# Performance work log

Hardware: AMD Instinct MI355X
Metric: run time of the kernel (lower is better)

Reference implementation:

```python
import jax, jax.numpy as jnp
import numpy as np

B, T, D = 4, 2048, 2048
H = 16
KD = D // 2          # key_dim = expand_k * d_model
VD = D               # value_dim = expand_v * d_model
DK = KD // H         # head_k_dim = 64
DV = VD // H         # head_v_dim = 128
LR = 16              # gate_low_rank_dim
EPS = 1e-5
GATE_LOGIT_NORMALIZER = 16.0


def setup_inputs() -> dict:
    key = jax.random.key(0)
    ks = jax.random.split(key, 9)
    def w(k, shape):
        fan_in = shape[0]
        return (jax.random.normal(k, shape, jnp.float32) * (fan_in ** -0.5)).astype(jnp.float32)
    return {
        "x":      jax.random.normal(ks[0], (B, T, D), jnp.float32),
        "Wq":     w(ks[1], (D, KD)),
        "Wk":     w(ks[2], (D, KD)),
        "Wv":     w(ks[3], (D, VD)),
        "Wg":     w(ks[4], (D, VD)),      # output gate projection
        "Wgk1":   w(ks[5], (D, LR)),      # gk low-rank down-proj (no bias)
        "Wgk2":   w(ks[6], (LR, KD)),     # gk up-proj
        "bgk2":   jnp.zeros((KD,), jnp.float32),
        "norm_w": jnp.ones((DV,), jnp.float32),  # per-head RMSNorm weight
        "Wo":     w(ks[7], (VD, D)),
    }


def reference(x, Wq, Wk, Wv, Wg, Wgk1, Wgk2, bgk2, norm_w, Wo):
    b, t, _ = x.shape
    dv = norm_w.shape[0]
    vd = Wv.shape[1]
    h = vd // dv
    dk = Wq.shape[1] // h
    scale = dk ** -0.5

    q = (x @ Wq).reshape(b, t, h, dk) * scale
    k = (x @ Wk).reshape(b, t, h, dk)
    v = (x @ Wv).reshape(b, t, h, dv)
    # forget gate: logsigmoid(low_rank_proj(x)) / gate_logit_normalizer
    gk = jax.nn.log_sigmoid((x @ Wgk1) @ Wgk2 + bgk2) / GATE_LOGIT_NORMALIZER
    gk = gk.reshape(b, t, h, dk)

    # time-major for scan: [T, B, H, d]
    qT = jnp.moveaxis(q, 1, 0)
    kT = jnp.moveaxis(k, 1, 0)
    vT = jnp.moveaxis(v, 1, 0)
    gT = jnp.moveaxis(gk, 1, 0)

    def step(S, inp):
        qt, kt, vt, gt = inp
        # S_t = diag(exp(gk_t)) S_{t-1} + k_t^T v_t ; shape [B,H,DK,DV]
        S = S * jnp.exp(gt)[..., None] + kt[..., None] * vt[..., None, :]
        ot = jnp.einsum('bhk,bhkv->bhv', qt, S)
        return S, ot

    S0 = jnp.zeros((b, h, dk, dv), x.dtype)
    _, o = jax.lax.scan(step, S0, (qT, kT, vT, gT))
    o = jnp.moveaxis(o, 0, 1)  # [B, T, H, DV]

    # FusedRMSNormSwishGate: rmsnorm(o) * weight * swish(g), per head dim
    g = (x @ Wg).reshape(b, t, h, dv)
    o = o * jax.lax.rsqrt(jnp.mean(o * o, axis=-1, keepdims=True) + EPS) * norm_w
    o = o * (g * jax.nn.sigmoid(g))
    return o.reshape(b, t, vd) @ Wo
```

## Files before the change

kernel.cpp:

```cpp
#include <hip/hip_runtime.h>
#include <hip/hip_bf16.h>
#include <type_traits>


using bf16x8 = __attribute__((ext_vector_type(8))) short;
using f32x4  = __attribute__((ext_vector_type(4))) float;

static __device__ __forceinline__ float bf2f(ushort u) {
  union { unsigned int i; float f; } v;
  v.i = ((unsigned int)u) << 16;
  return v.f;
}
static __device__ __forceinline__ ushort f2bf(float f) {
  __hip_bfloat16 h = __float2bfloat16(f);
  return *reinterpret_cast<ushort*>(&h);
}
static __device__ __forceinline__ unsigned int pack2(float lo, float hi) {
  return (unsigned int)f2bf(lo) | ((unsigned int)f2bf(hi) << 16);
}
static __device__ __forceinline__ void unpack8(uint4 v, float* f) {
  f[0] = bf2f((ushort)(v.x & 0xffff)); f[1] = bf2f((ushort)(v.x >> 16));
  f[2] = bf2f((ushort)(v.y & 0xffff)); f[3] = bf2f((ushort)(v.y >> 16));
  f[4] = bf2f((ushort)(v.z & 0xffff)); f[5] = bf2f((ushort)(v.z >> 16));
  f[6] = bf2f((ushort)(v.w & 0xffff)); f[7] = bf2f((ushort)(v.w >> 16));
}

#define GLDS16(g, l) __builtin_amdgcn_global_load_lds( \
    (const __attribute__((address_space(1))) unsigned int*)(g), \
    (__attribute__((address_space(3))) unsigned int*)(l), 16, 0, 0)

#define SWZ3(row) ((((row) & 1) << 2) | (((row) >> 1) & 3))

__global__ __launch_bounds__(256) void f32_to_bf16(
    const float* __restrict__ in, ushort* __restrict__ out, long n) {
  long i = ((long)blockIdx.x * 256 + threadIdx.x) * 8;
  if (i >= n) return;
  float4 a = *(const float4*)(in + i);
  float4 b = *(const float4*)(in + i + 4);
  uint4 o;
  o.x = pack2(a.x, a.y); o.y = pack2(a.z, a.w);
  o.z = pack2(b.x, b.y); o.w = pack2(b.z, b.w);
  *(uint4*)(out + i) = o;
}

__global__ __launch_bounds__(256) void transpose_f32_bf16(
    const float* __restrict__ in, ushort* __restrict__ out, int R, int C) {
  __shared__ float tile[64][65];
  const int t = threadIdx.x;
  const int tc = blockIdx.x * 64;
  const int tr = blockIdx.y * 64;
  const int lr = t >> 2;
  const int lc = (t & 3) * 16;
  const float* ip = in + (long)(tr + lr) * C + tc + lc;
#pragma unroll
  for (int j = 0; j < 4; ++j)
    *(float4*)(&tile[lr][lc + j * 4]) = *(const float4*)(ip + j * 4);
  __syncthreads();
  const int c = t >> 2;
  const int r0 = (t & 3) * 16;
  ushort tmp[16];
#pragma unroll
  for (int j = 0; j < 16; ++j) tmp[j] = f2bf(tile[r0 + j][c]);
  ushort* op = out + (long)(tc + c) * R + tr + r0;
  *(uint4*)(op)     = *(uint4*)(tmp);
  *(uint4*)(op + 8) = *(uint4*)(tmp + 8);
}

template <typename OT>
__global__ __launch_bounds__(512, 2) void gemm_bt8(
    const ushort* __restrict__ A, const ushort* __restrict__ BT,
    OT* __restrict__ C, int M, int N, int K) {
  __shared__ ushort sA[2 * 16384];
  __shared__ ushort sB[2 * 16384];
  const int t = threadIdx.x;
  const int nbx = N >> 8;
  const int cpx = gridDim.x >> 3;
  const int wg = ((int)blockIdx.x & 7) * cpx + ((int)blockIdx.x >> 3);
  const int brow = (wg / nbx) * 256;
  const int bcol = (wg % nbx) * 256;

  const int w = t >> 6, l = t & 63;
  const int wm = w >> 2, wn = w & 3;
  const int lr = l & 15, lk = l >> 4;
  const int NT = K >> 6;

  const int srow = t >> 3;
  const int cswz = ((t & 7) ^ SWZ3(srow)) * 8;
  const ushort* Abase = A + (size_t)(brow + srow) * K + cswz;
  const ushort* Bbase = BT + (size_t)(bcol + srow) * K + cswz;
  const int t8 = t * 8;

  auto stageA = [&](int bb, int hh, int jt) {
    const ushort* s = Abase + (size_t)(hh * 128) * K + jt * 64;
    ushort* d = sA + bb * 16384 + hh * 8192 + t8;
    GLDS16(s, d);
    GLDS16(s + (size_t)64 * K, d + 4096);
  };
  auto stageB = [&](int bb, int hh, int jt) {
    const ushort* s = Bbase + (size_t)(hh * 128) * K + jt * 64;
    ushort* d = sB + bb * 16384 + hh * 8192 + t8;
    GLDS16(s, d);
    GLDS16(s + (size_t)64 * K, d + 4096);
  };

  const int swz = SWZ3(lr);
  const int ks0 = ((0 + lk) ^ swz) * 8;
  const int ks1 = ((4 + lk) ^ swz) * 8;
  const int aRd = (wm * 16 + lr) * 64;
  const int bRd = (wn * 16 + lr) * 64;

  f32x4 acc[8][4];
#pragma unroll
  for (int m = 0; m < 8; ++m)
#pragma unroll
    for (int n = 0; n < 4; ++n) acc[m][n] = (f32x4){0.f, 0.f, 0.f, 0.f};

  stageA(0, 0, 0); stageB(0, 0, 0); stageB(0, 1, 0); stageA(0, 1, 0);
  asm volatile("s_waitcnt vmcnt(4)" ::: "memory");
  stageA(1, 0, 1); stageB(1, 0, 1); stageB(1, 1, 1);
  asm volatile("s_waitcnt vmcnt(6)" ::: "memory");
  __builtin_amdgcn_s_barrier();

  for (int kt = 0; kt < NT; ++kt) {
    const int bb = kt & 1;
    const int aOff = bb * 16384, bOff = bb * 16384;
    bf16x8 aF[4][2], bF[2][2][2];

#pragma unroll
    for (int m = 0; m < 4; ++m) {
      aF[m][0] = *(const bf16x8*)(sA + aOff + aRd + m * 2048 + ks0);
      aF[m][1] = *(const bf16x8*)(sA + aOff + aRd + m * 2048 + ks1);
    }
#pragma unroll
    for (int n = 0; n < 2; ++n) {
      bF[0][n][0] = *(const bf16x8*)(sB + bOff + bRd + n * 4096 + ks0);
      bF[0][n][1] = *(const bf16x8*)(sB + bOff + bRd + n * 4096 + ks1);
    }
    if (kt + 1 < NT) stageA(bb ^ 1, 1, kt + 1);
    __builtin_amdgcn_s_barrier();
    __builtin_amdgcn_s_setprio(1);
#pragma unroll
    for (int m = 0; m < 4; ++m)
#pragma unroll
      for (int n = 0; n < 2; ++n) {
        acc[m][n] = __builtin_amdgcn_mfma_f32_16x16x32_bf16(aF[m][0], bF[0][n][0], acc[m][n], 0, 0, 0);
        acc[m][n] = __builtin_amdgcn_mfma_f32_16x16x32_bf16(aF[m][1], bF[0][n][1], acc[m][n], 0, 0, 0);
      }
    __builtin_amdgcn_s_setprio(0);
    __builtin_amdgcn_s_barrier();

#pragma unroll
    for (int n = 0; n < 2; ++n) {
      bF[1][n][0] = *(const bf16x8*)(sB + bOff + 8192 + bRd + n * 4096 + ks0);
      bF[1][n][1] = *(const bf16x8*)(sB + bOff + 8192 + bRd + n * 4096 + ks1);
    }
    if (kt + 2 < NT) stageA(bb, 0, kt + 2);
    __builtin_amdgcn_s_barrier();
    __builtin_amdgcn_s_setprio(1);
#pragma unroll
    for (int m = 0; m < 4; ++m)
#pragma unroll
      for (int n = 0; n < 2; ++n) {
        acc[m][2 + n] = __builtin_amdgcn_mfma_f32_16x16x32_bf16(aF[m][0], bF[1][n][0], acc[m][2 + n], 0, 0, 0);
        acc[m][2 + n] = __builtin_amdgcn_mfma_f32_16x16x32_bf16(aF[m][1], bF[1][n][1], acc[m][2 + n], 0, 0, 0);
      }
    __builtin_amdgcn_s_setprio(0);
    __builtin_amdgcn_s_barrier();

#pragma unroll
    for (int m = 0; m < 4; ++m) {
      aF[m][0] = *(const bf16x8*)(sA + aOff + 8192 + aRd + m * 2048 + ks0);
      aF[m][1] = *(const bf16x8*)(sA + aOff + 8192 + aRd + m * 2048 + ks1);
    }
    if (kt + 2 < NT) stageB(bb, 0, kt + 2);
    __builtin_amdgcn_s_barrier();
    __builtin_amdgcn_s_setprio(1);
#pragma unroll
    for (int m = 0; m < 4; ++m)
#pragma unroll
      for (int n = 0; n < 2; ++n) {
        acc[4 + m][n] = __builtin_amdgcn_mfma_f32_16x16x32_bf16(aF[m][0], bF[0][n][0], acc[4 + m][n], 0, 0, 0);
        acc[4 + m][n] = __builtin_amdgcn_mfma_f32_16x16x32_bf16(aF[m][1], bF[0][n][1], acc[4 + m][n], 0, 0, 0);
      }
    __builtin_amdgcn_s_setprio(0);
    __builtin_amdgcn_s_barrier();

    if (kt + 2 < NT) stageB(bb, 1, kt + 2);
    __builtin_amdgcn_s_barrier();
    __builtin_amdgcn_s_setprio(1);
#pragma unroll
    for (int m = 0; m < 4; ++m)
#pragma unroll
      for (int n = 0; n < 2; ++n) {
        acc[4 + m][2 + n] = __builtin_amdgcn_mfma_f32_16x16x32_bf16(aF[m][0], bF[1][n][0], acc[4 + m][2 + n], 0, 0, 0);
        acc[4 + m][2 + n] = __builtin_amdgcn_mfma_f32_16x16x32_bf16(aF[m][1], bF[1][n][1], acc[4 + m][2 + n], 0, 0, 0);
      }
    __builtin_amdgcn_s_setprio(0);
    if (kt < NT - 2)       asm volatile("s_waitcnt vmcnt(6)" ::: "memory");
    else if (kt == NT - 2) asm volatile("s_waitcnt vmcnt(0)" ::: "memory");
    __builtin_amdgcn_s_barrier();
  }

  const int rq = lk * 4;
#pragma unroll
  for (int mq = 0; mq < 8; ++mq)
#pragma unroll
    for (int nq = 0; nq < 4; ++nq) {
      long row = brow + mq * 32 + wm * 16 + rq;
      long col = bcol + nq * 64 + wn * 16 + lr;
      OT* cp = C + row * N + col;
#pragma unroll
      for (int r = 0; r < 4; ++r) {
        if constexpr (std::is_same_v<OT, ushort>) cp[(long)r * N] = f2bf(acc[mq][nq][r]);
        else                                      cp[(long)r * N] = acc[mq][nq][r];
      }
    }
}

__global__ __launch_bounds__(256) void gate_kernel(
    const float* __restrict__ x, const float* __restrict__ Wgk1,
    const float* __restrict__ Wgk2, const float* __restrict__ bgk2,
    ushort* __restrict__ gbuf) {
  const int m = blockIdx.x;
  const int t = threadIdx.x;
  __shared__ float sx[2048];
  __shared__ float red[256];
  __shared__ float z1[16];
  const float* xr = x + (long)m * 2048;
  *(float4*)(sx + t * 8)     = *(const float4*)(xr + t * 8);
  *(float4*)(sx + t * 8 + 4) = *(const float4*)(xr + t * 8 + 4);
  __syncthreads();
  const int j = t & 15, seg = t >> 4;
  float s = 0.f;
  for (int d = 0; d < 128; ++d)
    s += sx[seg * 128 + d] * Wgk1[(seg * 128 + d) * 16 + j];
  red[t] = s;
  __syncthreads();
  if (t < 16) {
    float z = 0.f;
    for (int sg = 0; sg < 16; ++sg) z += red[sg * 16 + t];
    z1[t] = z;
  }
  __syncthreads();
#pragma unroll
  for (int r = 0; r < 4; ++r) {
    int n = r * 256 + t;
    float a = bgk2[n];
#pragma unroll
    for (int l2 = 0; l2 < 16; ++l2) a += z1[l2] * Wgk2[l2 * 1024 + n];
    float ls = fminf(a, 0.f) - log1pf(__expf(-fabsf(a)));
    gbuf[(long)m * 1024 + n] = f2bf(ls * 0.0625f);
  }
}

__global__ __launch_bounds__(256) void chunk_contrib_kernel(
    const ushort* __restrict__ qkvg, const ushort* __restrict__ gbuf,
    float* __restrict__ Sall, float* __restrict__ Gtot) {
  const int blk = blockIdx.x;
  const int bh = blk >> 5, c = blk & 31;
  const int b = bh >> 4, h = bh & 15;
  const long row0 = (long)b * 2048 + c * 64;
  const int th = threadIdx.x;

  __shared__ float  gc[64][65];
  __shared__ ushort khT[64][72];
  __shared__ ushort vT[128][72];

  {
    const int t = th >> 2;
    const int k0 = (th & 3) * 16;
    const ushort* gp = gbuf + (row0 + t) * 1024 + h * 64 + k0;
    uint4 a = *(const uint4*)gp;
    uint4 b4 = *(const uint4*)(gp + 8);
    float f[8];
    unpack8(a, f);
#pragma unroll
    for (int j = 0; j < 8; ++j) gc[t][k0 + j] = f[j];
    unpack8(b4, f);
#pragma unroll
    for (int j = 0; j < 8; ++j) gc[t][k0 + 8 + j] = f[j];
  }
  __syncthreads();
  if (th < 64) {
    float s = 0.f;
    for (int t = 0; t < 64; ++t) { s += gc[t][th]; gc[t][th] = s; }
  }
  __syncthreads();
  if (th < 64) Gtot[(long)blk * 64 + th] = gc[63][th];

  {
    const int s = th & 63, kq = th >> 6;
    const ushort* kp = qkvg + (row0 + s) * 6144 + 1024 + h * 64 + kq * 16;
    uint4 a = *(const uint4*)kp;
    uint4 b4 = *(const uint4*)(kp + 8);
    float f[16];
    unpack8(a, f); unpack8(b4, f + 8);
#pragma unroll
    for (int j = 0; j < 16; ++j) {
      int k = kq * 16 + j;
      khT[k][s] = f2bf(f[j] * __expf(gc[63][k] - gc[s][k]));
    }
    const ushort* vp = qkvg + (row0 + s) * 6144 + 2048 + h * 128 + kq * 32;
#pragma unroll
    for (int u = 0; u < 4; ++u) {
      uint4 vv = *(const uint4*)(vp + u * 8);
      const ushort* pv = (const ushort*)&vv;
#pragma unroll
      for (int j = 0; j < 8; ++j) vT[kq * 32 + u * 8 + j][s] = pv[j];
    }
  }
  __syncthreads();

  const int w = th >> 6, l = th & 63;
  const int lr = l & 15, kq8 = (l >> 4) * 8;
  f32x4 acc[4][2];
#pragma unroll
  for (int m = 0; m < 4; ++m)
#pragma unroll
    for (int n = 0; n < 2; ++n) acc[m][n] = (f32x4){0.f, 0.f, 0.f, 0.f};
#pragma unroll
  for (int ks = 0; ks < 64; ks += 32) {
#pragma unroll
    for (int m = 0; m < 4; ++m) {
      bf16x8 af = *(const bf16x8*)(&khT[m * 16 + lr][ks + kq8]);
#pragma unroll
      for (int n = 0; n < 2; ++n) {
        bf16x8 bv = *(const bf16x8*)(&vT[w * 32 + n * 16 + lr][ks + kq8]);
        acc[m][n] = __builtin_amdgcn_mfma_f32_16x16x32_bf16(af, bv, acc[m][n], 0, 0, 0);
      }
    }
  }
  float* Cc = Sall + (long)blk * 8192;
  const int rq = (l >> 4) * 4;
#pragma unroll
  for (int m = 0; m < 4; ++m)
#pragma unroll
    for (int n = 0; n < 2; ++n) {
      int k = m * 16 + rq;
      int dv = w * 32 + n * 16 + lr;
#pragma unroll
      for (int r = 0; r < 4; ++r) Cc[(k + r) * 128 + dv] = acc[m][n][r];
    }
}

__global__ __launch_bounds__(256) void chunk_scan_kernel(
    float* __restrict__ Sall, const float* __restrict__ Gtot) {
  const int blk = blockIdx.x;
  const int bh = blk >> 2, qd = blk & 3;
  const int th = threadIdx.x;
  const int k = th >> 2;
  const int dv = qd * 32 + (th & 3) * 8;
  float* base = Sall + (long)bh * 32 * 8192 + k * 128 + dv;
  const float* gt = Gtot + (long)bh * 32 * 64 + k;
  float S[8];
#pragma unroll
  for (int i = 0; i < 8; ++i) S[i] = 0.f;
  for (int c = 0; c < 32; ++c) {
    float4 c0 = *(const float4*)(base);
    float4 c1 = *(const float4*)(base + 4);
    float eg = __expf(gt[c * 64]);
    float4 s0 = {S[0], S[1], S[2], S[3]};
    float4 s1 = {S[4], S[5], S[6], S[7]};
    *(float4*)(base) = s0;
    *(float4*)(base + 4) = s1;
    S[0] = S[0] * eg + c0.x; S[1] = S[1] * eg + c0.y;
    S[2] = S[2] * eg + c0.z; S[3] = S[3] * eg + c0.w;
    S[4] = S[4] * eg + c1.x; S[5] = S[5] * eg + c1.y;
    S[6] = S[6] * eg + c1.z; S[7] = S[7] * eg + c1.w;
    base += 8192;
  }
}

__global__ __launch_bounds__(256) void chunk_output_kernel(
    const ushort* __restrict__ qkvg, const ushort* __restrict__ gbuf,
    const float* __restrict__ Sall, const float* __restrict__ norm_w,
    ushort* __restrict__ oo) {
  const int blk = blockIdx.x;
  const int bh = blk >> 5, c = blk & 31;
  const int b = bh >> 4, h = bh & 15;
  const long row0 = (long)b * 2048 + c * 64;
  const int th = threadIdx.x;

  __shared__ float  gc[64][65];
  __shared__ ushort qg[64][72];
  __shared__ ushort kg[64][72];
  __shared__ ushort vT[128][72];
  __shared__ ushort ST[128][72];
  __shared__ ushort P[64][72];
  __shared__ ushort ot[64][136];

  {
    const int t = th >> 2;
    const int s4 = (th & 3);
    const int k0 = s4 * 16;
    const ushort* gp = gbuf + (row0 + t) * 1024 + h * 64 + k0;
    uint4 a = *(const uint4*)gp;
    uint4 b4 = *(const uint4*)(gp + 8);
    float f[8];
    unpack8(a, f);
#pragma unroll
    for (int j = 0; j < 8; ++j) gc[t][k0 + j] = f[j];
    unpack8(b4, f);
#pragma unroll
    for (int j = 0; j < 8; ++j) gc[t][k0 + 8 + j] = f[j];

    const ushort* qp = qkvg + (row0 + t) * 6144 + h * 64 + k0;
    *(uint4*)(&qg[t][k0])     = *(const uint4*)qp;
    *(uint4*)(&qg[t][k0 + 8]) = *(const uint4*)(qp + 8);
    const ushort* kp = qp + 1024;
    *(uint4*)(&kg[t][k0])     = *(const uint4*)kp;
    *(uint4*)(&kg[t][k0 + 8]) = *(const uint4*)(kp + 8);

    const ushort* gtp = qkvg + (row0 + t) * 6144 + 4096 + h * 128 + s4 * 32;
#pragma unroll
    for (int u = 0; u < 4; ++u)
      *(uint4*)(&ot[t][s4 * 32 + u * 8]) = *(const uint4*)(gtp + u * 8);
  }
  {
    const int s = th & 63, kq = th >> 6;
    const ushort* vp = qkvg + (row0 + s) * 6144 + 2048 + h * 128 + kq * 32;
#pragma unroll
    for (int u = 0; u < 4; ++u) {
      uint4 vv = *(const uint4*)(vp + u * 8);
      const ushort* pv = (const ushort*)&vv;
#pragma unroll
      for (int j = 0; j < 8; ++j) vT[kq * 32 + u * 8 + j][s] = pv[j];
    }
  }
  {
    const int k = th >> 2;
    const int dvb = (th & 3) * 32;
    const float* sp = Sall + (long)blk * 8192 + k * 128 + dvb;
#pragma unroll
    for (int u = 0; u < 8; ++u) {
      float4 sv = *(const float4*)(sp + u * 4);
      ST[dvb + u * 4 + 0][k] = f2bf(sv.x);
      ST[dvb + u * 4 + 1][k] = f2bf(sv.y);
      ST[dvb + u * 4 + 2][k] = f2bf(sv.z);
      ST[dvb + u * 4 + 3][k] = f2bf(sv.w);
    }
  }
  __syncthreads();
  if (th < 64) {
    float s = 0.f;
    for (int t = 0; t < 64; ++t) { s += gc[t][th]; gc[t][th] = s; }
  }
  __syncthreads();
  {
    const int t = th & 63, kb = (th >> 6) * 16;
#pragma unroll
    for (int u = 0; u < 2; ++u) {
      uint4 qv = *(const uint4*)(&qg[t][kb + u * 8]);
      uint4 kv = *(const uint4*)(&kg[t][kb + u * 8]);
      float qf[8], kf[8];
      unpack8(qv, qf); unpack8(kv, kf);
      ushort qo[8], ko[8];
#pragma unroll
      for (int j = 0; j < 8; ++j) {
        float g = gc[t][kb + u * 8 + j];
        qo[j] = f2bf(qf[j] * __expf(g) * 0.125f);
        ko[j] = f2bf(kf[j] * __expf(-g));
      }
      *(uint4*)(&qg[t][kb + u * 8]) = *(uint4*)qo;
      *(uint4*)(&kg[t][kb + u * 8]) = *(uint4*)ko;
    }
  }
  __syncthreads();

  const int w = th >> 6, l = th & 63;
  const int lr = l & 15, kq8 = (l >> 4) * 8;
  const int rq = (l >> 4) * 4;

  f32x4 acc1[4];
#pragma unroll
  for (int n = 0; n < 4; ++n) acc1[n] = (f32x4){0.f, 0.f, 0.f, 0.f};
#pragma unroll
  for (int kk = 0; kk < 64; kk += 32) {
    bf16x8 af = *(const bf16x8*)(&qg[w * 16 + lr][kk + kq8]);
#pragma unroll
    for (int n = 0; n < 4; ++n) {
      bf16x8 bv = *(const bf16x8*)(&kg[n * 16 + lr][kk + kq8]);
      acc1[n] = __builtin_amdgcn_mfma_f32_16x16x32_bf16(af, bv, acc1[n], 0, 0, 0);
    }
  }
#pragma unroll
  for (int n = 0; n < 4; ++n) {
    int s = n * 16 + lr;
#pragma unroll
    for (int r = 0; r < 4; ++r) {
      int t = w * 16 + rq + r;
      P[t][s] = f2bf(s <= t ? acc1[n][r] : 0.f);
    }
  }
  __syncthreads();

  f32x4 acc2[8];
#pragma unroll
  for (int n = 0; n < 8; ++n) acc2[n] = (f32x4){0.f, 0.f, 0.f, 0.f};
#pragma unroll
  for (int ks = 0; ks < 64; ks += 32) {
    bf16x8 af = *(const bf16x8*)(&P[w * 16 + lr][ks + kq8]);
#pragma unroll
    for (int n = 0; n < 8; ++n) {
      bf16x8 bv = *(const bf16x8*)(&vT[n * 16 + lr][ks + kq8]);
      acc2[n] = __builtin_amdgcn_mfma_f32_16x16x32_bf16(af, bv, acc2[n], 0, 0, 0);
    }
  }
#pragma unroll
  for (int kk = 0; kk < 64; kk += 32) {
    bf16x8 af = *(const bf16x8*)(&qg[w * 16 + lr][kk + kq8]);
#pragma unroll
    for (int n = 0; n < 8; ++n) {
      bf16x8 bv = *(const bf16x8*)(&ST[n * 16 + lr][kk + kq8]);
      acc2[n] = __builtin_amdgcn_mfma_f32_16x16x32_bf16(af, bv, acc2[n], 0, 0, 0);
    }
  }

  float sumsq[4] = {0.f, 0.f, 0.f, 0.f};
#pragma unroll
  for (int n = 0; n < 8; ++n)
#pragma unroll
    for (int r = 0; r < 4; ++r) sumsq[r] += acc2[n][r] * acc2[n][r];
#pragma unroll
  for (int d = 1; d < 16; d <<= 1)
#pragma unroll
    for (int r = 0; r < 4; ++r) sumsq[r] += __shfl_xor(sumsq[r], d);
  float inv[4];
#pragma unroll
  for (int r = 0; r < 4; ++r) inv[r] = rsqrtf(sumsq[r] * (1.f / 128.f) + 1e-5f);

#pragma unroll
  for (int n = 0; n < 8; ++n) {
    int dv = n * 16 + lr;
    float nw = norm_w[dv];
#pragma unroll
    for (int r = 0; r < 4; ++r) {
      int t = w * 16 + rq + r;
      float g = bf2f(ot[t][dv]);
      float sw = g / (1.f + __expf(-g));
      ot[t][dv] = f2bf(acc2[n][r] * inv[r] * nw * sw);
    }
  }
  __syncthreads();

  {
    const int row = th >> 2;
    const int col0 = (th & 3) * 32;
    ushort* op = oo + (row0 + row) * 2048 + h * 128 + col0;
#pragma unroll
    for (int u = 0; u < 4; ++u)
      *(uint4*)(op + u * 8) = *(const uint4*)(&ot[row][col0 + u * 8]);
  }
}

extern "C" void kernel_launch(void* const* d_in, const int* in_sizes, int n_in,
                              void* d_out, int out_size, void* d_ws, size_t ws_size,
                              hipStream_t stream) {
  const float* x      = (const float*)d_in[0];
  const float* Wq     = (const float*)d_in[1];
  const float* Wk     = (const float*)d_in[2];
  const float* Wv     = (const float*)d_in[3];
  const float* Wg     = (const float*)d_in[4];
  const float* Wgk1   = (const float*)d_in[5];
  const float* Wgk2   = (const float*)d_in[6];
  const float* bgk2   = (const float*)d_in[7];
  const float* norm_w = (const float*)d_in[8];
  const float* Wo     = (const float*)d_in[9];
  float* out = (float*)d_out;

  char* ws = (char*)d_ws;
  ushort* WT   = (ushort*)(ws);
  ushort* WoT  = (ushort*)(ws + 25165824);
  ushort* qkvg = (ushort*)(ws + 33554432);
  ushort* gbuf = (ushort*)(ws + 134217728);
  float*  Sall = (float*)(ws + 150994944);
  ushort* xb   = (ushort*)(ws + 150994944);
  float*  Gtot = (float*)(ws + 218103808);
  ushort* oo   = (ushort*)(ws + 218628096);

  dim3 blk(256);
  f32_to_bf16<<<dim3(8192), blk, 0, stream>>>(x, xb, (long)8192 * 2048);
  transpose_f32_bf16<<<dim3(16, 32), blk, 0, stream>>>(Wq, WT, 2048, 1024);
  transpose_f32_bf16<<<dim3(16, 32), blk, 0, stream>>>(Wk, WT + (size_t)1024 * 2048, 2048, 1024);
  transpose_f32_bf16<<<dim3(32, 32), blk, 0, stream>>>(Wv, WT + (size_t)2048 * 2048, 2048, 2048);
  transpose_f32_bf16<<<dim3(32, 32), blk, 0, stream>>>(Wg, WT + (size_t)4096 * 2048, 2048, 2048);
  transpose_f32_bf16<<<dim3(32, 32), blk, 0, stream>>>(Wo, WoT, 2048, 2048);

  gemm_bt8<ushort><<<dim3(768), dim3(512), 0, stream>>>(xb, WT, qkvg, 8192, 6144, 2048);
  gate_kernel<<<dim3(8192), blk, 0, stream>>>(x, Wgk1, Wgk2, bgk2, gbuf);

  chunk_contrib_kernel<<<dim3(2048), blk, 0, stream>>>(qkvg, gbuf, Sall, Gtot);
  chunk_scan_kernel<<<dim3(256), blk, 0, stream>>>(Sall, Gtot);
  chunk_output_kernel<<<dim3(2048), blk, 0, stream>>>(qkvg, gbuf, Sall, norm_w, oo);

  gemm_bt8<float><<<dim3(256), dim3(512), 0, stream>>>(oo, WoT, out, 8192, 2048, 2048);
}
```

Measured before the change: 523.7 us.

## Switch GEMM to 32x32 MFMA, store chunk states as transposed bf16, trim output kernel

Result: faster. 476.2 us (-9.1%).

```diff
diff --git a/kernel.cpp b/kernel.cpp
--- a/kernel.cpp
+++ b/kernel.cpp
@@ -5,6 +5,7 @@
 
 using bf16x8 = __attribute__((ext_vector_type(8))) short;
 using f32x4  = __attribute__((ext_vector_type(4))) float;
+using f32x16 = __attribute__((ext_vector_type(16))) float;
 
 static __device__ __forceinline__ float bf2f(ushort u) {
   union { unsigned int i; float f; } v;
@@ -81,7 +82,7 @@
 
   const int w = t >> 6, l = t & 63;
   const int wm = w >> 2, wn = w & 3;
-  const int lr = l & 15, lk = l >> 4;
+  const int l31 = l & 31, l5 = l >> 5;
   const int NT = K >> 6;
 
   const int srow = t >> 3;
@@ -103,17 +104,18 @@
     GLDS16(s + (size_t)64 * K, d + 4096);
   };
 
-  const int swz = SWZ3(lr);
-  const int ks0 = ((0 + lk) ^ swz) * 8;
-  const int ks1 = ((4 + lk) ^ swz) * 8;
-  const int aRd = (wm * 16 + lr) * 64;
-  const int bRd = (wn * 16 + lr) * 64;
-
-  f32x4 acc[8][4];
-#pragma unroll
-  for (int m = 0; m < 8; ++m)
-#pragma unroll
-    for (int n = 0; n < 4; ++n) acc[m][n] = (f32x4){0.f, 0.f, 0.f, 0.f};
+  const int swz = SWZ3(l31 & 7);
+  const int aRow = (wm * 32 + l31) * 64;
+  const int bRow = (wn * 32 + l31) * 64;
+#define KSL(ks) ((((ks) * 2 + l5) ^ swz) * 8)
+
+  f32x16 acc[4][2];
+#pragma unroll
+  for (int m = 0; m < 4; ++m)
+#pragma unroll
+    for (int n = 0; n < 2; ++n)
+#pragma unroll
+      for (int r = 0; r < 16; ++r) acc[m][n][r] = 0.f;
 
   stageA(0, 0, 0); stageB(0, 0, 0); stageB(0, 1, 0); stageA(0, 1, 0);
   asm volatile("s_waitcnt vmcnt(4)" ::: "memory");
@@ -124,64 +126,54 @@
   for (int kt = 0; kt < NT; ++kt) {
     const int bb = kt & 1;
     const int aOff = bb * 16384, bOff = bb * 16384;
-    bf16x8 aF[4][2], bF[2][2][2];
-
-#pragma unroll
-    for (int m = 0; m < 4; ++m) {
-      aF[m][0] = *(const bf16x8*)(sA + aOff + aRd + m * 2048 + ks0);
-      aF[m][1] = *(const bf16x8*)(sA + aOff + aRd + m * 2048 + ks1);
-    }
-#pragma unroll
-    for (int n = 0; n < 2; ++n) {
-      bF[0][n][0] = *(const bf16x8*)(sB + bOff + bRd + n * 4096 + ks0);
-      bF[0][n][1] = *(const bf16x8*)(sB + bOff + bRd + n * 4096 + ks1);
-    }
+    bf16x8 aF[2][4], bF[2][4];
+
+#pragma unroll
+    for (int mf = 0; mf < 2; ++mf)
+#pragma unroll
+      for (int ks = 0; ks < 4; ++ks)
+        aF[mf][ks] = *(const bf16x8*)(sA + aOff + mf * 4096 + aRow + KSL(ks));
+#pragma unroll
+    for (int ks = 0; ks < 4; ++ks)
+      bF[0][ks] = *(const bf16x8*)(sB + bOff + bRow + KSL(ks));
     if (kt + 1 < NT) stageA(bb ^ 1, 1, kt + 1);
     __builtin_amdgcn_s_barrier();
     __builtin_amdgcn_s_setprio(1);
 #pragma unroll
-    for (int m = 0; m < 4; ++m)
-#pragma unroll
-      for (int n = 0; n < 2; ++n) {
-        acc[m][n] = __builtin_amdgcn_mfma_f32_16x16x32_bf16(aF[m][0], bF[0][n][0], acc[m][n], 0, 0, 0);
-        acc[m][n] = __builtin_amdgcn_mfma_f32_16x16x32_bf16(aF[m][1], bF[0][n][1], acc[m][n], 0, 0, 0);
-      }
+    for (int mf = 0; mf < 2; ++mf)
+#pragma unroll
+      for (int ks = 0; ks < 4; ++ks)
+        acc[mf][0] = __builtin_amdgcn_mfma_f32_32x32x16_bf16(aF[mf][ks], bF[0][ks], acc[mf][0], 0, 0, 0);
     __builtin_amdgcn_s_setprio(0);
     __builtin_amdgcn_s_barrier();
 
 #pragma unroll
-    for (int n = 0; n < 2; ++n) {
-      bF[1][n][0] = *(const bf16x8*)(sB + bOff + 8192 + bRd + n * 4096 + ks0);
-      bF[1][n][1] = *(const bf16x8*)(sB + bOff + 8192 + bRd + n * 4096 + ks1);
-    }
+    for (int ks = 0; ks < 4; ++ks)
+      bF[1][ks] = *(const bf16x8*)(sB + bOff + 8192 + bRow + KSL(ks));
     if (kt + 2 < NT) stageA(bb, 0, kt + 2);
     __builtin_amdgcn_s_barrier();
     __builtin_amdgcn_s_setprio(1);
 #pragma unroll
-    for (int m = 0; m < 4; ++m)
-#pragma unroll
-      for (int n = 0; n < 2; ++n) {
-        acc[m][2 + n] = __builtin_amdgcn_mfma_f32_16x16x32_bf16(aF[m][0], bF[1][n][0], acc[m][2 + n], 0, 0, 0);
-        acc[m][2 + n] = __builtin_amdgcn_mfma_f32_16x16x32_bf16(aF[m][1], bF[1][n][1], acc[m][2 + n], 0, 0, 0);
-      }
+    for (int mf = 0; mf < 2; ++mf)
+#pragma unroll
+      for (int ks = 0; ks < 4; ++ks)
+        acc[mf][1] = __builtin_amdgcn_mfma_f32_32x32x16_bf16(aF[mf][ks], bF[1][ks], acc[mf][1], 0, 0, 0);
     __builtin_amdgcn_s_setprio(0);
     __builtin_amdgcn_s_barrier();
 
 #pragma unroll
-    for (int m = 0; m < 4; ++m) {
-      aF[m][0] = *(const bf16x8*)(sA + aOff + 8192 + aRd + m * 2048 + ks0);
-      aF[m][1] = *(const bf16x8*)(sA + aOff + 8192 + aRd + m * 2048 + ks1);
-    }
+    for (int mf = 0; mf < 2; ++mf)
+#pragma unroll
+      for (int ks = 0; ks < 4; ++ks)
+        aF[mf][ks] = *(const bf16x8*)(sA + aOff + 8192 + mf * 4096 + aRow + KSL(ks));
     if (kt + 2 < NT) stageB(bb, 0, kt + 2);
     __builtin_amdgcn_s_barrier();
     __builtin_amdgcn_s_setprio(1);
 #pragma unroll
-    for (int m = 0; m < 4; ++m)
-#pragma unroll
-      for (int n = 0; n < 2; ++n) {
-        acc[4 + m][n] = __builtin_amdgcn_mfma_f32_16x16x32_bf16(aF[m][0], bF[0][n][0], acc[4 + m][n], 0, 0, 0);
-        acc[4 + m][n] = __builtin_amdgcn_mfma_f32_16x16x32_bf16(aF[m][1], bF[0][n][1], acc[4 + m][n], 0, 0, 0);
-      }
+    for (int mf = 0; mf < 2; ++mf)
+#pragma unroll
+      for (int ks = 0; ks < 4; ++ks)
+        acc[2 + mf][0] = __builtin_amdgcn_mfma_f32_32x32x16_bf16(aF[mf][ks], bF[0][ks], acc[2 + mf][0], 0, 0, 0);
     __builtin_amdgcn_s_setprio(0);
     __builtin_amdgcn_s_barrier();
 
@@ -189,36 +181,34 @@
     __builtin_amdgcn_s_barrier();
     __builtin_amdgcn_s_setprio(1);
 #pragma unroll
-    for (int m = 0; m < 4; ++m)
-#pragma unroll
-      for (int n = 0; n < 2; ++n) {
-        acc[4 + m][2 + n] = __builtin_amdgcn_mfma_f32_16x16x32_bf16(aF[m][0], bF[1][n][0], acc[4 + m][2 + n], 0, 0, 0);
-        acc[4 + m][2 + n] = __builtin_amdgcn_mfma_f32_16x16x32_bf16(aF[m][1], bF[1][n][1], acc[4 + m][2 + n], 0, 0, 0);
-      }
+    for (int mf = 0; mf < 2; ++mf)
+#pragma unroll
+      for (int ks = 0; ks < 4; ++ks)
+        acc[2 + mf][1] = __builtin_amdgcn_mfma_f32_32x32x16_bf16(aF[mf][ks], bF[1][ks], acc[2 + mf][1], 0, 0, 0);
     __builtin_amdgcn_s_setprio(0);
     if (kt < NT - 2)       asm volatile("s_waitcnt vmcnt(6)" ::: "memory");
     else if (kt == NT - 2) asm volatile("s_waitcnt vmcnt(0)" ::: "memory");
     __builtin_amdgcn_s_barrier();
   }
-
-  const int rq = lk * 4;
-#pragma unroll
-  for (int mq = 0; mq < 8; ++mq)
-#pragma unroll
-    for (int nq = 0; nq < 4; ++nq) {
-      long row = brow + mq * 32 + wm * 16 + rq;
-      long col = bcol + nq * 64 + wn * 16 + lr;
-      OT* cp = C + row * N + col;
-#pragma unroll
-      for (int r = 0; r < 4; ++r) {
-        if constexpr (std::is_same_v<OT, ushort>) cp[(long)r * N] = f2bf(acc[mq][nq][r]);
-        else                                      cp[(long)r * N] = acc[mq][nq][r];
+#undef KSL
+
+#pragma unroll
+  for (int mf = 0; mf < 4; ++mf)
+#pragma unroll
+    for (int nf = 0; nf < 2; ++nf) {
+      long col = bcol + nf * 128 + wn * 32 + l31;
+      long rbase = brow + mf * 64 + wm * 32 + 4 * l5;
+#pragma unroll
+      for (int r = 0; r < 16; ++r) {
+        long row = rbase + (r & 3) + 8 * (r >> 2);
+        if constexpr (std::is_same_v<OT, ushort>) C[row * N + col] = f2bf(acc[mf][nf][r]);
+        else                                      C[row * N + col] = acc[mf][nf][r];
       }
     }
 }
 
 __global__ __launch_bounds__(256) void gate_kernel(
-    const float* __restrict__ x, const float* __restrict__ Wgk1,
+    const ushort* __restrict__ xb, const float* __restrict__ Wgk1,
     const float* __restrict__ Wgk2, const float* __restrict__ bgk2,
     ushort* __restrict__ gbuf) {
   const int m = blockIdx.x;
@@ -226,9 +216,14 @@
   __shared__ float sx[2048];
   __shared__ float red[256];
   __shared__ float z1[16];
-  const float* xr = x + (long)m * 2048;
-  *(float4*)(sx + t * 8)     = *(const float4*)(xr + t * 8);
-  *(float4*)(sx + t * 8 + 4) = *(const float4*)(xr + t * 8 + 4);
+  const ushort* xr = xb + (long)m * 2048;
+  {
+    uint4 v = *(const uint4*)(xr + t * 8);
+    float f[8];
+    unpack8(v, f);
+#pragma unroll
+    for (int j = 0; j < 8; ++j) sx[t * 8 + j] = f[j];
+  }
   __syncthreads();
   const int j = t & 15, seg = t >> 4;
   float s = 0.f;
@@ -255,7 +250,7 @@
 
 __global__ __launch_bounds__(256) void chunk_contrib_kernel(
     const ushort* __restrict__ qkvg, const ushort* __restrict__ gbuf,
-    float* __restrict__ Sall, float* __restrict__ Gtot) {
+    ushort* __restrict__ STbuf, float* __restrict__ EGtot) {
   const int blk = blockIdx.x;
   const int bh = blk >> 5, c = blk & 31;
   const int b = bh >> 4, h = bh & 15;
@@ -286,7 +281,7 @@
     for (int t = 0; t < 64; ++t) { s += gc[t][th]; gc[t][th] = s; }
   }
   __syncthreads();
-  if (th < 64) Gtot[(long)blk * 64 + th] = gc[63][th];
+  if (th < 64) EGtot[(long)blk * 64 + th] = __expf(gc[63][th]);
 
   {
     const int s = th & 63, kq = th >> 6;
@@ -330,50 +325,61 @@
       }
     }
   }
-  float* Cc = Sall + (long)blk * 8192;
+  ushort* Cc = STbuf + (long)blk * 8192;
   const int rq = (l >> 4) * 4;
 #pragma unroll
   for (int m = 0; m < 4; ++m)
 #pragma unroll
     for (int n = 0; n < 2; ++n) {
-      int k = m * 16 + rq;
       int dv = w * 32 + n * 16 + lr;
-#pragma unroll
-      for (int r = 0; r < 4; ++r) Cc[(k + r) * 128 + dv] = acc[m][n][r];
+      ushort tmp[4];
+#pragma unroll
+      for (int r = 0; r < 4; ++r) tmp[r] = f2bf(acc[m][n][r]);
+      *(uint2*)(Cc + dv * 64 + m * 16 + rq) = *(uint2*)tmp;
     }
 }
 
 __global__ __launch_bounds__(256) void chunk_scan_kernel(
-    float* __restrict__ Sall, const float* __restrict__ Gtot) {
+    ushort* __restrict__ STbuf, const float* __restrict__ EGtot) {
   const int blk = blockIdx.x;
   const int bh = blk >> 2, qd = blk & 3;
   const int th = threadIdx.x;
-  const int k = th >> 2;
-  const int dv = qd * 32 + (th & 3) * 8;
-  float* base = Sall + (long)bh * 32 * 8192 + k * 128 + dv;
-  const float* gt = Gtot + (long)bh * 32 * 64 + k;
+  const int dv = qd * 32 + (th >> 3);
+  const int k0 = (th & 7) * 8;
+  ushort* base = STbuf + (long)bh * 32 * 8192 + dv * 64 + k0;
+  const float* eg = EGtot + (long)bh * 32 * 64 + k0;
   float S[8];
 #pragma unroll
   for (int i = 0; i < 8; ++i) S[i] = 0.f;
+  uint4 cv = *(const uint4*)base;
+  float4 e0 = *(const float4*)(eg);
+  float4 e1 = *(const float4*)(eg + 4);
   for (int c = 0; c < 32; ++c) {
-    float4 c0 = *(const float4*)(base);
-    float4 c1 = *(const float4*)(base + 4);
-    float eg = __expf(gt[c * 64]);
-    float4 s0 = {S[0], S[1], S[2], S[3]};
-    float4 s1 = {S[4], S[5], S[6], S[7]};
-    *(float4*)(base) = s0;
-    *(float4*)(base + 4) = s1;
-    S[0] = S[0] * eg + c0.x; S[1] = S[1] * eg + c0.y;
-    S[2] = S[2] * eg + c0.z; S[3] = S[3] * eg + c0.w;
-    S[4] = S[4] * eg + c1.x; S[5] = S[5] * eg + c1.y;
-    S[6] = S[6] * eg + c1.z; S[7] = S[7] * eg + c1.w;
-    base += 8192;
+    ushort* cur = base;
+    base += 8192; eg += 64;
+    uint4 nv = cv; float4 n0 = e0, n1 = e1;
+    if (c < 31) {
+      nv = *(const uint4*)base;
+      n0 = *(const float4*)(eg);
+      n1 = *(const float4*)(eg + 4);
+    }
+    float cf[8];
+    unpack8(cv, cf);
+    float ee[8] = {e0.x, e0.y, e0.z, e0.w, e1.x, e1.y, e1.z, e1.w};
+    ushort so[8];
+#pragma unroll
+    for (int i = 0; i < 8; ++i) {
+      so[i] = f2bf(S[i]);
+      S[i] = S[i] * ee[i] + cf[i];
+    }
+    *(uint4*)cur = *(uint4*)so;
+    cv = nv; e0 = n0; e1 = n1;
   }
 }
 
 __global__ __launch_bounds__(256) void chunk_output_kernel(
     const ushort* __restrict__ qkvg, const ushort* __restrict__ gbuf,
-    const float* __restrict__ Sall, const float* __restrict__ norm_w,
+    const ushort* __restrict__ STbuf, const float* __restrict__ norm_w,
     ushort* __restrict__ oo) {
   const int blk = blockIdx.x;
   const int bh = blk >> 5, c = blk & 31;
@@ -381,18 +387,17 @@
   const long row0 = (long)b * 2048 + c * 64;
   const int th = threadIdx.x;
 
-  __shared__ float  gc[64][65];
-  __shared__ ushort qg[64][72];
-  __shared__ ushort kg[64][72];
-  __shared__ ushort vT[128][72];
-  __shared__ ushort ST[128][72];
-  __shared__ ushort P[64][72];
-  __shared__ ushort ot[64][136];
+  __shared__ __align__(16) char pool[71936];
+  float  (*gc)[65]  = (float(*)[65])(pool);
+  ushort (*qg)[72]  = (ushort(*)[72])(pool + 16640);
+  ushort (*kg)[72]  = (ushort(*)[72])(pool + 25856);
+  ushort (*vT)[72]  = (ushort(*)[72])(pool + 35072);
+  ushort (*STs)[72] = (ushort(*)[72])(pool + 53504);
+  ushort (*P)[72]   = (ushort(*)[72])(pool);
 
   {
     const int t = th >> 2;
-    const int s4 = (th & 3);
-    const int k0 = s4 * 16;
+    const int k0 = (th & 3) * 16;
     const ushort* gp = gbuf + (row0 + t) * 1024 + h * 64 + k0;
     uint4 a = *(const uint4*)gp;
     uint4 b4 = *(const uint4*)(gp + 8);
@@ -410,11 +415,6 @@
     const ushort* kp = qp + 1024;
     *(uint4*)(&kg[t][k0])     = *(const uint4*)kp;
     *(uint4*)(&kg[t][k0 + 8]) = *(const uint4*)(kp + 8);
-
-    const ushort* gtp = qkvg + (row0 + t) * 6144 + 4096 + h * 128 + s4 * 32;
-#pragma unroll
-    for (int u = 0; u < 4; ++u)
-      *(uint4*)(&ot[t][s4 * 32 + u * 8]) = *(const uint4*)(gtp + u * 8);
   }
   {
     const int s = th & 63, kq = th >> 6;
@@ -428,17 +428,12 @@
     }
   }
   {
-    const int k = th >> 2;
-    const int dvb = (th & 3) * 32;
-    const float* sp = Sall + (long)blk * 8192 + k * 128 + dvb;
-#pragma unroll
-    for (int u = 0; u < 8; ++u) {
-      float4 sv = *(const float4*)(sp + u * 4);
-      ST[dvb + u * 4 + 0][k] = f2bf(sv.x);
-      ST[dvb + u * 4 + 1][k] = f2bf(sv.y);
-      ST[dvb + u * 4 + 2][k] = f2bf(sv.z);
-      ST[dvb + u * 4 + 3][k] = f2bf(sv.w);
-    }
+    const int row = th >> 1;
+    const int col0 = (th & 1) * 32;
+    const ushort* sp = STbuf + (long)blk * 8192 + row * 64 + col0;
+#pragma unroll
+    for (int u = 0; u < 4; ++u)
+      *(uint4*)(&STs[row][col0 + u * 8]) = *(const uint4*)(sp + u * 8);
   }
   __syncthreads();
   if (th < 64) {
@@ -511,9 +506,18 @@
     bf16x8 af = *(const bf16x8*)(&qg[w * 16 + lr][kk + kq8]);
 #pragma unroll
     for (int n = 0; n < 8; ++n) {
-      bf16x8 bv = *(const bf16x8*)(&ST[n * 16 + lr][kk + kq8]);
+      bf16x8 bv = *(const bf16x8*)(&STs[n * 16 + lr][kk + kq8]);
       acc2[n] = __builtin_amdgcn_mfma_f32_16x16x32_bf16(af, bv, acc2[n], 0, 0, 0);
     }
+  }
+
+  float gv[8][4];
+#pragma unroll
+  for (int n = 0; n < 8; ++n) {
+    int dv = n * 16 + lr;
+#pragma unroll
+    for (int r = 0; r < 4; ++r)
+      gv[n][r] = bf2f(qkvg[(row0 + w * 16 + rq + r) * 6144 + 4096 + h * 128 + dv]);
   }
 
   float sumsq[4] = {0.f, 0.f, 0.f, 0.f};
@@ -535,21 +539,11 @@
     float nw = norm_w[dv];
 #pragma unroll
     for (int r = 0; r < 4; ++r) {
-      int t = w * 16 + rq + r;
-      float g = bf2f(ot[t][dv]);
+      float g = gv[n][r];
       float sw = g / (1.f + __expf(-g));
-      ot[t][dv] = f2bf(acc2[n][r] * inv[r] * nw * sw);
-    }
-  }
-  __syncthreads();
-
-  {
-    const int row = th >> 2;
-    const int col0 = (th & 3) * 32;
-    ushort* op = oo + (row0 + row) * 2048 + h * 128 + col0;
-#pragma unroll
-    for (int u = 0; u < 4; ++u)
-      *(uint4*)(op + u * 8) = *(const uint4*)(&ot[row][col0 + u * 8]);
+      oo[(row0 + w * 16 + rq + r) * 2048 + h * 128 + dv] =
+          f2bf(acc2[n][r] * inv[r] * nw * sw);
+    }
   }
 }
 
@@ -569,14 +563,14 @@
   float* out = (float*)d_out;
 
   char* ws = (char*)d_ws;
-  ushort* WT   = (ushort*)(ws);
-  ushort* WoT  = (ushort*)(ws + 25165824);
-  ushort* qkvg = (ushort*)(ws + 33554432);
-  ushort* gbuf = (ushort*)(ws + 134217728);
-  float*  Sall = (float*)(ws + 150994944);
-  ushort* xb   = (ushort*)(ws + 150994944);
-  float*  Gtot = (float*)(ws + 218103808);
-  ushort* oo   = (ushort*)(ws + 218628096);
+  ushort* WT    = (ushort*)(ws);
+  ushort* WoT   = (ushort*)(ws + 25165824);
+  ushort* qkvg  = (ushort*)(ws + 33554432);
+  ushort* gbuf  = (ushort*)(ws + 134217728);
+  ushort* STbuf = (ushort*)(ws + 150994944);
+  ushort* xb    = (ushort*)(ws + 150994944);
+  float*  EGtot = (float*)(ws + 184549376);
+  ushort* oo    = (ushort*)(ws + 185073664);
 
   dim3 blk(256);
   f32_to_bf16<<<dim3(8192), blk, 0, stream>>>(x, xb, (long)8192 * 2048);
@@ -587,11 +581,11 @@
   transpose_f32_bf16<<<dim3(32, 32), blk, 0, stream>>>(Wo, WoT, 2048, 2048);
 
   gemm_bt8<ushort><<<dim3(768), dim3(512), 0, stream>>>(xb, WT, qkvg, 8192, 6144, 2048);
-  gate_kernel<<<dim3(8192), blk, 0, stream>>>(x, Wgk1, Wgk2, bgk2, gbuf);
-
-  chunk_contrib_kernel<<<dim3(2048), blk, 0, stream>>>(qkvg, gbuf, Sall, Gtot);
-  chunk_scan_kernel<<<dim3(256), blk, 0, stream>>>(Sall, Gtot);
-  chunk_output_kernel<<<dim3(2048), blk, 0, stream>>>(qkvg, gbuf, Sall, norm_w, oo);
+  gate_kernel<<<dim3(8192), blk, 0, stream>>>(xb, Wgk1, Wgk2, bgk2, gbuf);
+
+  chunk_contrib_kernel<<<dim3(2048), blk, 0, stream>>>(qkvg, gbuf, STbuf, EGtot);
+  chunk_scan_kernel<<<dim3(256), blk, 0, stream>>>(STbuf, EGtot);
+  chunk_output_kernel<<<dim3(2048), blk, 0, stream>>>(qkvg, gbuf, STbuf, norm_w, oo);
 
   gemm_bt8<float><<<dim3(256), dim3(512), 0, stream>>>(oo, WoT, out, 8192, 2048, 2048);
 }
```
